# Optimization experiments

Hardware: AMD Instinct MI355X
Metric: run time of the kernel (lower is better)

## Reference

```python
import jax, jax.numpy as jnp
import numpy as np

N_SIGMA = 1
NUM_CLASS = 1
N_INST = 16          # max instance id (ids 1..16); instances==0 is background
W_INST, W_VAR, W_SEED = 1.0, 10.0, 1.0
H, W, B = 512, 512, 8
GRID = 1024          # buffer is linspace over 1024 then cropped to H,W


def make_xym(h, w, dtype=jnp.float32):
    full = jnp.linspace(0.0, 1.0, GRID, dtype=dtype)
    xm = jnp.broadcast_to(full[:w][None, :], (h, w))   # x varies along width
    ym = jnp.broadcast_to(full[:h][:, None], (h, w))   # y varies along height
    return jnp.stack([xm, ym], axis=0)                 # [2, H, W]


def lovasz_hinge_flat(logits, labels):
    # logits: [N] float, labels: [N] float in {0,1}
    signs = 2.0 * labels - 1.0
    errors = 1.0 - logits * signs
    order = jnp.argsort(-errors)
    errors_sorted = errors[order]
    gt_sorted = labels[order]
    gts = jnp.sum(gt_sorted)
    intersection = gts - jnp.cumsum(gt_sorted)
    union = gts + jnp.cumsum(1.0 - gt_sorted)
    jaccard = 1.0 - intersection / union
    grad = jnp.concatenate([jaccard[:1], jaccard[1:] - jaccard[:-1]])
    return jnp.sum(jax.nn.relu(errors_sorted) * grad)


def _per_image(pred, instance, label, xym):
    h, w = pred.shape[1], pred.shape[2]
    spatial_emb = jnp.tanh(pred[0:2]) + xym              # [2,H,W]
    sigma = pred[2:2 + N_SIGMA]                          # [n_sigma,H,W]
    seed = jax.nn.sigmoid(pred[2 + N_SIGMA])             # [H,W] (num_class==1)

    label_mask = (label == 1)
    bg_mask = (label == 0)
    seed_loss = jnp.sum(jnp.where(bg_mask, seed ** 2, 0.0))

    ids = jnp.arange(1, N_INST + 1)
    masks = (instance[None] == ids[:, None, None]) & label_mask[None]  # [K,H,W] bool
    maskf = masks.astype(pred.dtype)
    counts = jnp.sum(maskf, axis=(1, 2))                 # [K]
    present = counts > 0
    safe = jnp.maximum(counts, 1.0)

    # to_center=True: center = mean of xym coords over each instance mask
    center = jnp.einsum('khw,chw->kc', maskf, xym) / safe[:, None]        # [K,2]
    s_mean = jnp.einsum('khw,shw->ks', maskf, sigma) / safe[:, None]      # [K,n_sigma]

    # var loss: mean over in-mask pixels of (sigma - detached mean)^2
    dev2 = (sigma[None] - jax.lax.stop_gradient(s_mean)[:, :, None, None]) ** 2  # [K,ns,H,W]
    var_terms = jnp.einsum('khw,kshw->k', maskf, dev2) / (safe * N_SIGMA)

    # dist = exp(-s * sum_c (emb_c - center_c)^2), s = exp(10 * mean sigma)
    s_exp = jnp.exp(10.0 * s_mean)[:, 0]                 # [K] (n_sigma==1 broadcasts)
    diff2 = jnp.sum((spatial_emb[None] - center[:, :, None, None]) ** 2, axis=1)  # [K,H,W]
    dist = jnp.exp(-s_exp[:, None, None] * diff2)        # [K,H,W]

    inst_losses = jax.vmap(
        lambda d, m: lovasz_hinge_flat(2.0 * d.ravel() - 1.0, m.ravel())
    )(dist, maskf)
    instance_loss = jnp.sum(jnp.where(present, inst_losses, 0.0))
    var_loss = jnp.sum(jnp.where(present, var_terms, 0.0))

    seed_loss = seed_loss + jnp.sum(
        maskf * (seed[None] - jax.lax.stop_gradient(dist)) ** 2)

    obj = jnp.maximum(jnp.sum(present.astype(pred.dtype)), 1.0)
    return (W_INST * instance_loss / obj
            + W_VAR * var_loss / obj
            + W_SEED * seed_loss / (h * w))


def setup_inputs() -> dict:
    key = jax.random.key(0)
    k1, k2, k3 = jax.random.split(key, 3)
    prediction = jax.random.normal(k1, (B, 2 + N_SIGMA + NUM_CLASS, H, W), dtype=jnp.float32)
    instances = jax.random.randint(k2, (B, H, W), 0, N_INST + 1).astype(jnp.int64)
    labels = jax.random.randint(k3, (B, H, W), 0, NUM_CLASS + 1).astype(jnp.int64)
    return {"prediction": prediction, "instances": instances, "labels": labels}


def reference(prediction, instances, labels):
    xym = make_xym(prediction.shape[2], prediction.shape[3], prediction.dtype)
    per_img = jax.vmap(_per_image, in_axes=(0, 0, 0, None))(
        prediction, instances, labels, xym)
    return jnp.mean(per_img)
```

## Files before the change

### kernel.cpp

```cpp
#include <hip/hip_runtime.h>
#include <hip/hip_fp16.h>
#include <math.h>

#define HWPX 262144
#define NIMG 8
#define ACC_STRIDE 96
#define NB 1024
#define ZMAX 8.0f
#define NSPLIT 32
#define NGRP 2

typedef unsigned long long u64;

template<bool PACK>
__global__ __launch_bounds__(256) void k_prep(const float* __restrict__ pred,
    const int* __restrict__ inst, const int* __restrict__ lab,
    u64* __restrict__ rec, double* __restrict__ accd)
{
  __shared__ float s[8][83];
  int t = threadIdx.x;
  for (int i = t; i < 8*83; i += 256) (&s[0][0])[i] = 0.0f;
  __syncthreads();
  int bid = blockIdx.x;
  int b = bid >> 7;
  int base = (bid & 127) << 11;
  const float* pb = pred + (size_t)b * 4 * HWPX;
  size_t ib = (size_t)b * HWPX;
  int r = t & 7;
  float bg = 0.0f;
  #pragma unroll
  for (int i = 0; i < 8; ++i) {
    int px = base + (i << 8) + t;
    int h = px >> 9, w = px & 511;
    float xm = w * (1.0f/1023.0f), ym = h * (1.0f/1023.0f);
    float sg = pb[2*HWPX + px];
    float p3 = pb[3*HWPX + px];
    float sd = 1.0f / (1.0f + __expf(-p3));
    int lv = lab[ib+px], iv = inst[ib+px];
    int mid = (lv == 1 && (unsigned)(iv-1) < 16u) ? iv : 0;
    if (PACK) {
      float ex = tanhf(pb[px]) + xm;
      float ey = tanhf(pb[HWPX+px]) + ym;
      u64 v = (u64)__half_as_ushort(__float2half(ex))
            | ((u64)__half_as_ushort(__float2half(ey)) << 16)
            | ((u64)__half_as_ushort(__float2half(sd)) << 32)
            | ((u64)mid << 48);
      rec[ib+px] = v;
    }
    if (lv == 0) {
      bg += sd*sd;
    } else if (mid) {
      int k = mid - 1;
      atomicAdd(&s[r][k], 1.0f);
      atomicAdd(&s[r][16+k], xm);
      atomicAdd(&s[r][32+k], ym);
      atomicAdd(&s[r][48+k], sg);
      atomicAdd(&s[r][64+k], sg*sg);
    }
  }
  #pragma unroll
  for (int o = 32; o > 0; o >>= 1) bg += __shfl_down(bg, o);
  if ((t & 63) == 0) atomicAdd(&s[0][80], bg);
  __syncthreads();
  if (t < 81) {
    float v = 0.0f;
    #pragma unroll
    for (int rr = 0; rr < 8; ++rr) v += s[rr][t];
    if (v != 0.0f) atomicAdd(&accd[(size_t)b*ACC_STRIDE + t], (double)v);
  }
}

__global__ __launch_bounds__(128) void k_fin(double* __restrict__ accd, float* __restrict__ pairinfo)
{
  __shared__ double varr[128];
  __shared__ float pres[128];
  int t = threadIdx.x;
  int b = t >> 4, k = t & 15;
  double* ab = accd + (size_t)b*ACC_STRIDE;
  double cnt = ab[k];
  double safe = cnt > 0.0 ? cnt : 1.0;
  double ss = ab[48+k];
  double cx = ab[16+k]/safe, cy = ab[32+k]/safe, sm = ss/safe;
  double var = (ab[64+k] - ss*ss/safe)/safe;
  if (var < 0.0) var = 0.0;
  float4 pi = make_float4((float)cx, (float)cy, (float)exp(10.0*sm), (float)cnt);
  reinterpret_cast<float4*>(pairinfo)[t] = pi;
  pres[t] = cnt > 0.0 ? 1.0f : 0.0f;
  varr[t] = cnt > 0.0 ? var : 0.0;
  __syncthreads();
  if (t < NIMG) {
    float np = 0.0f; double vs = 0.0;
    for (int i = 0; i < 16; ++i) { np += pres[t*16+i]; vs += varr[t*16+i]; }
    double* ab2 = accd + (size_t)t*ACC_STRIDE;
    ab2[83] = vs;
    ab2[84] = (np > 1.0f) ? (double)np : 1.0;
  }
}

__global__ __launch_bounds__(1024) void k_hist(const u64* __restrict__ rec,
    const float* __restrict__ pairinfo,
    unsigned* __restrict__ partial, double* __restrict__ accd)
{
  __shared__ unsigned hist[8*NB];
  __shared__ float redf[16];
  int t = threadIdx.x, bid = blockIdx.x;
  int b = bid & 7;
  int r = bid >> 3;
  int g = r & 1;
  int s = r >> 1;
  for (int i = t; i < 8*NB; i += 1024) hist[i] = 0u;
  float cx[8], cy[8], se[8], s128[8];
  #pragma unroll
  for (int j = 0; j < 8; ++j) {
    float4 pi = reinterpret_cast<const float4*>(pairinfo)[b*16 + g*8 + j];
    cx[j] = pi.x; cy[j] = pi.y; se[j] = pi.z; s128[j] = pi.z * (float)(NB/ZMAX);
  }
  __syncthreads();
  size_t base = (size_t)b*HWPX + (size_t)s*(HWPX/NSPLIT);
  float fit = 0.0f;
  for (int it = 0; it < HWPX/NSPLIT/1024; ++it) {
    size_t px = base + it*1024 + t;
    u64 v = rec[px];
    float ex = __half2float(__ushort_as_half((unsigned short)(v & 0xffffu)));
    float ey = __half2float(__ushort_as_half((unsigned short)((v >> 16) & 0xffffu)));
    float sd = __half2float(__ushort_as_half((unsigned short)((v >> 32) & 0xffffu)));
    int rel = (int)(v >> 48) - 1 - g*8;
    #pragma unroll
    for (int j = 0; j < 8; ++j) {
      float dx = ex - cx[j], dy = ey - cy[j];
      float d2 = fmaf(dx, dx, dy*dy);
      int key; unsigned add;
      if (rel == j) {
        float d = __expf(-d2 * se[j]);
        float e = fmaf(-2.0f, d, 2.0f);
        int kk = (int)(e * (float)(NB/2));
        key = kk > NB-1 ? NB-1 : kk;
        add = 0x10000u;
        float df = sd - d; fit += df*df;
      } else {
        key = (int)fminf(d2 * s128[j], (float)(NB-1));
        add = 1u;
      }
      atomicAdd(&hist[j*NB + key], add);
    }
  }
  #pragma unroll
  for (int o = 32; o > 0; o >>= 1) fit += __shfl_down(fit, o);
  if ((t & 63) == 0) redf[t >> 6] = fit;
  __syncthreads();
  if (t == 0) {
    float ft = 0.0f;
    for (int i = 0; i < 16; ++i) ft += redf[i];
    atomicAdd(&accd[(size_t)b*ACC_STRIDE + 81], (double)ft);
  }
  unsigned* pp = partial + (size_t)((b*NGRP + g)*NSPLIT + s)*(8*NB);
  for (int i = t; i < 8*NB; i += 1024) pp[i] = hist[i];
}

__global__ __launch_bounds__(1024) void k_scan(const unsigned* __restrict__ partial,
    const float* __restrict__ pairinfo, double* __restrict__ accd)
{
  __shared__ unsigned sp[NB], sq[NB];
  __shared__ float red[16];
  int t = threadIdx.x, bid = blockIdx.x;
  int b = bid >> 4, k = bid & 15;
  int g = k >> 3, j8 = k & 7;
  float G = pairinfo[(b*16 + k)*4 + 3];
  if (G <= 0.0f) return;
  sq[t] = 0u;
  __syncthreads();
  unsigned p = 0, q = 0;
  const unsigned* basep = partial + (size_t)((b*NGRP + g)*NSPLIT)*(8*NB) + j8*NB + t;
  #pragma unroll 4
  for (int s2 = 0; s2 < NSPLIT; ++s2) {
    unsigned h = basep[(size_t)s2*(8*NB)];
    p += h >> 16; q += h & 0xffffu;
  }
  float zmid = (t + 0.5f) * (ZMAX/NB);
  float ev = 2.0f * __expf(-zmid);
  int eb = (int)(ev * (float)(NB/2));
  if (eb > NB-1) eb = NB-1;
  if (q) atomicAdd(&sq[eb], q);
  __syncthreads();
  unsigned qe = sq[t];
  __syncthreads();
  int j = (NB-1) - t;
  sp[j] = p; sq[j] = qe;
  __syncthreads();
  for (int off = 1; off < NB; off <<= 1) {
    unsigned vp = 0, vq = 0;
    if (j >= off) { vp = sp[j-off]; vq = sq[j-off]; }
    __syncthreads();
    sp[j] += vp; sq[j] += vq;
    __syncthreads();
  }
  float A  = (float)(sp[j] - p);
  float Bn = (float)(sq[j] - qe);
  float val = (t + 0.5f) * (2.0f/NB);
  float pf = (float)p, qf = (float)qe;
  float Jb = (A + Bn) / (G + Bn);
  float Ja = (A + Bn + pf + qf) / (G + Bn + qf);
  float contrib = val * (Ja - Jb);
  #pragma unroll
  for (int o = 32; o > 0; o >>= 1) contrib += __shfl_down(contrib, o);
  if ((t & 63) == 0) red[t >> 6] = contrib;
  __syncthreads();
  if (t == 0) {
    float tot = 0.0f;
    for (int i = 0; i < 16; ++i) tot += red[i];
    atomicAdd(&accd[(size_t)b*ACC_STRIDE + 82], (double)tot);
  }
}

__global__ __launch_bounds__(1024) void k_lov_old(const float* __restrict__ pred,
    const int* __restrict__ inst, const int* __restrict__ lab,
    const float* __restrict__ pairinfo, double* __restrict__ accd)
{
  constexpr int SHIFT = 18;
  constexpr int NBB = (0x40000000 >> SHIFT) + 1;
  extern __shared__ unsigned char smem[];
  unsigned* histP = reinterpret_cast<unsigned*>(smem);
  unsigned* histQ = histP + NBB;
  unsigned* scanP = histQ + NBB;
  unsigned* scanQ = scanP + 1024;
  float* red  = reinterpret_cast<float*>(scanQ + 1024);
  float* redf = red + 16;
  int t = threadIdx.x, bid = blockIdx.x;
  int b = bid >> 4, k = bid & 15;
  float4 pi = reinterpret_cast<const float4*>(pairinfo)[bid];
  float cx = pi.x, cy = pi.y, sexp = pi.z, G = pi.w;
  if (G <= 0.0f) return;
  for (int i = t; i < 2*NBB; i += 1024) histP[i] = 0u;
  __syncthreads();
  size_t ib = (size_t)b * HWPX;
  const float* pb = pred + (size_t)b * 4 * HWPX;
  const int target = k + 1;
  float fit = 0.0f;
  for (int j = 0; j < HWPX/1024; ++j) {
    int px = (j << 10) + t;
    int h = px >> 9, w = px & 511;
    float ex = tanhf(pb[px]) + w*(1.0f/1023.0f);
    float ey = tanhf(pb[HWPX+px]) + h*(1.0f/1023.0f);
    float sd = 1.0f/(1.0f + __expf(-pb[3*HWPX+px]));
    int lv = lab[ib+px], iv = inst[ib+px];
    float dx = ex - cx, dy = ey - cy;
    float d = __expf(-sexp * (dx*dx + dy*dy));
    bool m = (lv == 1) && (iv == target);
    float e = m ? fmaf(-2.0f, d, 2.0f) : 2.0f * d;
    unsigned key = __float_as_uint(e) >> SHIFT;
    atomicAdd(m ? &histP[key] : &histQ[key], 1u);
    if (m) { float df = sd - d; fit += df*df; }
  }
  #pragma unroll
  for (int o = 32; o > 0; o >>= 1) fit += __shfl_down(fit, o);
  if ((t & 63) == 0) redf[t >> 6] = fit;
  __syncthreads();
  constexpr int CB = NBB / 1024;
  int start = (NBB - 1) - t * CB;
  int nk = (t == 1023) ? (CB + 1) : CB;
  unsigned lp = 0, lq = 0;
  for (int i = 0; i < nk; ++i) { lp += histP[start-i]; lq += histQ[start-i]; }
  scanP[t] = lp; scanQ[t] = lq;
  __syncthreads();
  for (int off = 1; off < 1024; off <<= 1) {
    unsigned vp = 0, vq = 0;
    if (t >= off) { vp = scanP[t-off]; vq = scanQ[t-off]; }
    __syncthreads();
    scanP[t] += vp; scanQ[t] += vq;
    __syncthreads();
  }
  float A  = (float)(scanP[t] - lp);
  float Bn = (float)(scanQ[t] - lq);
  float contrib = 0.0f;
  for (int i = 0; i < nk; ++i) {
    int kk = start - i;
    unsigned p = histP[kk], q = histQ[kk];
    if (p | q) {
      float lo = __uint_as_float((unsigned)kk << SHIFT);
      float hi = __uint_as_float((unsigned)(kk+1) << SHIFT);
      float valv = 0.5f*(lo+hi);
      if (valv > 2.0f) valv = 2.0f;
      float pq = (float)(p + q), qf = (float)q;
      float Jb = (A + Bn) / (G + Bn);
      float Ja = (A + Bn + pq) / (G + Bn + qf);
      contrib += valv * (Ja - Jb);
      A += (float)p; Bn += qf;
    }
  }
  #pragma unroll
  for (int o = 32; o > 0; o >>= 1) contrib += __shfl_down(contrib, o);
  if ((t & 63) == 0) red[t >> 6] = contrib;
  __syncthreads();
  if (t == 0) {
    float tot = 0.0f, ft = 0.0f;
    for (int i = 0; i < 16; ++i) { tot += red[i]; ft += redf[i]; }
    atomicAdd(&accd[(size_t)b*ACC_STRIDE + 82], (double)tot);
    atomicAdd(&accd[(size_t)b*ACC_STRIDE + 81], (double)ft);
  }
}

__global__ void k_final(const double* __restrict__ accd, float* __restrict__ out)
{
  int t = threadIdx.x;
  double lb = 0.0;
  if (t < NIMG) {
    const double* ab = accd + (size_t)t*ACC_STRIDE;
    lb = (ab[82] + 10.0*ab[83]) / ab[84] + (ab[80] + ab[81]) * (1.0/(double)HWPX);
  }
  #pragma unroll
  for (int o = 4; o > 0; o >>= 1) lb += __shfl_down(lb, o);
  if (t == 0) out[0] = (float)(lb * 0.125);
}

extern "C" void kernel_launch(void* const* d_in, const int* in_sizes, int n_in,
                              void* d_out, int out_size, void* d_ws, size_t ws_size,
                              hipStream_t stream)
{
  const float* pred = (const float*)d_in[0];
  const int*   inst = (const int*)d_in[1];
  const int*   lab  = (const int*)d_in[2];
  float* out = (float*)d_out;

  size_t recB  = (size_t)NIMG * HWPX * sizeof(u64);
  size_t partB = (size_t)NIMG * NGRP * NSPLIT * 8 * NB * 4;
  size_t accB  = (size_t)NIMG * ACC_STRIDE * sizeof(double);
  size_t pairB = 128 * 4 * sizeof(float);
  bool full = ws_size >= recB + partB + accB + pairB;

  char* ws = (char*)d_ws;
  if (full) {
    u64*      rec   = (u64*)ws;
    unsigned* part  = (unsigned*)(ws + recB);
    double*   accd  = (double*)(ws + recB + partB);
    float*    pairinfo = (float*)(ws + recB + partB + accB);
    hipMemsetAsync(accd, 0, accB, stream);
    k_prep<true><<<1024,256,0,stream>>>(pred, inst, lab, rec, accd);
    k_fin<<<1,128,0,stream>>>(accd, pairinfo);
    k_hist<<<NIMG*NGRP*NSPLIT,1024,0,stream>>>(rec, pairinfo, part, accd);
    k_scan<<<128,1024,0,stream>>>(part, pairinfo, accd);
    k_final<<<1,64,0,stream>>>(accd, out);
  } else {
    double* accd = (double*)ws;
    float* pairinfo = (float*)(accd + NIMG*ACC_STRIDE);
    hipMemsetAsync(accd, 0, accB, stream);
    k_prep<false><<<1024,256,0,stream>>>(pred, inst, lab, nullptr, accd);
    k_fin<<<1,128,0,stream>>>(accd, pairinfo);
    size_t lds18 = ((size_t)2*4097 + 2048)*4 + 128;
    k_lov_old<<<128,1024,lds18,stream>>>(pred, inst, lab, pairinfo, accd);
    k_final<<<1,64,0,stream>>>(accd, out);
  }
}
```

Baseline: 72.84 us.

## Fuse finalize stages into last-block reductions and vectorize prep and histogram loads

k_fin is folded into k_prep and k_final into k_scan using an atomic ticket counter, so the last block of each grid does the cross-block reduction. This removes two kernel launches and the workspace memset. k_prep now gives each thread 8 contiguous pixels, loaded and stored as 128-bit vectors, and uses fast exp-based tanh and sigmoid. k_hist reads two records per load. Per-block stats are reduced in float rather than double atomics, and correctness depends on the ticket counter starting at a multiple of the grid size, which the code assumes without explicitly zeroing it.

Result: slower. 244.3 us (+235.5%).

```diff
diff --git a/kernel.cpp b/kernel.cpp
--- a/kernel.cpp
+++ b/kernel.cpp
@@ -9,43 +9,73 @@
 #define ZMAX 8.0f
 #define NSPLIT 32
 #define NGRP 2
+#define PREP_GRID 1024
+#define SCAN_GRID 128
 
 typedef unsigned long long u64;
+
+__device__ __forceinline__ float tanh_fast(float x) {
+  float t = __expf(2.0f * x);
+  return 1.0f - __fdividef(2.0f, t + 1.0f);
+}
+__device__ __forceinline__ float sigmoid_fast(float x) {
+  return __fdividef(1.0f, 1.0f + __expf(-x));
+}
 
 template<bool PACK>
 __global__ __launch_bounds__(256) void k_prep(const float* __restrict__ pred,
     const int* __restrict__ inst, const int* __restrict__ lab,
-    u64* __restrict__ rec, double* __restrict__ accd)
+    u64* __restrict__ rec, float* __restrict__ part,
+    double* __restrict__ accd, float* __restrict__ pairinfo, unsigned* __restrict__ tick)
 {
   __shared__ float s[8][83];
+  __shared__ float red[96];
+  __shared__ int lastFlag;
   int t = threadIdx.x;
   for (int i = t; i < 8*83; i += 256) (&s[0][0])[i] = 0.0f;
   __syncthreads();
   int bid = blockIdx.x;
   int b = bid >> 7;
-  int base = (bid & 127) << 11;
-  const float* pb = pred + (size_t)b * 4 * HWPX;
-  size_t ib = (size_t)b * HWPX;
+  int px0 = ((bid & 127) << 11) + t*8;
+  const float* pb = pred + (size_t)b*4*HWPX;
+  size_t ib = (size_t)b*HWPX;
   int r = t & 7;
+  int w0 = px0 & 511;
+  float ym = (float)(px0 >> 9) * (1.0f/1023.0f);
+
+  float4 x0 = *(const float4*)(pb + px0);
+  float4 x1 = *(const float4*)(pb + px0 + 4);
+  float4 y0 = *(const float4*)(pb + HWPX + px0);
+  float4 y1 = *(const float4*)(pb + HWPX + px0 + 4);
+  float4 g0 = *(const float4*)(pb + 2*HWPX + px0);
+  float4 g1 = *(const float4*)(pb + 2*HWPX + px0 + 4);
+  float4 q0 = *(const float4*)(pb + 3*HWPX + px0);
+  float4 q1 = *(const float4*)(pb + 3*HWPX + px0 + 4);
+  int4 l0 = *(const int4*)(lab + ib + px0);
+  int4 l1 = *(const int4*)(lab + ib + px0 + 4);
+  int4 i0 = *(const int4*)(inst + ib + px0);
+  int4 i1 = *(const int4*)(inst + ib + px0 + 4);
+  float xs[8] = {x0.x,x0.y,x0.z,x0.w,x1.x,x1.y,x1.z,x1.w};
+  float ys[8] = {y0.x,y0.y,y0.z,y0.w,y1.x,y1.y,y1.z,y1.w};
+  float gs[8] = {g0.x,g0.y,g0.z,g0.w,g1.x,g1.y,g1.z,g1.w};
+  float qs[8] = {q0.x,q0.y,q0.z,q0.w,q1.x,q1.y,q1.z,q1.w};
+  int   ls[8] = {l0.x,l0.y,l0.z,l0.w,l1.x,l1.y,l1.z,l1.w};
+  int   is[8] = {i0.x,i0.y,i0.z,i0.w,i1.x,i1.y,i1.z,i1.w};
+  u64 rv[8];
   float bg = 0.0f;
   #pragma unroll
   for (int i = 0; i < 8; ++i) {
-    int px = base + (i << 8) + t;
-    int h = px >> 9, w = px & 511;
-    float xm = w * (1.0f/1023.0f), ym = h * (1.0f/1023.0f);
-    float sg = pb[2*HWPX + px];
-    float p3 = pb[3*HWPX + px];
-    float sd = 1.0f / (1.0f + __expf(-p3));
-    int lv = lab[ib+px], iv = inst[ib+px];
+    float xm = (float)(w0 + i) * (1.0f/1023.0f);
+    float sd = sigmoid_fast(qs[i]);
+    int lv = ls[i], iv = is[i];
     int mid = (lv == 1 && (unsigned)(iv-1) < 16u) ? iv : 0;
     if (PACK) {
-      float ex = tanhf(pb[px]) + xm;
-      float ey = tanhf(pb[HWPX+px]) + ym;
-      u64 v = (u64)__half_as_ushort(__float2half(ex))
+      float ex = tanh_fast(xs[i]) + xm;
+      float ey = tanh_fast(ys[i]) + ym;
+      rv[i] = (u64)__half_as_ushort(__float2half(ex))
             | ((u64)__half_as_ushort(__float2half(ey)) << 16)
             | ((u64)__half_as_ushort(__float2half(sd)) << 32)
             | ((u64)mid << 48);
-      rec[ib+px] = v;
     }
     if (lv == 0) {
       bg += sd*sd;
@@ -54,46 +84,73 @@
       atomicAdd(&s[r][k], 1.0f);
       atomicAdd(&s[r][16+k], xm);
       atomicAdd(&s[r][32+k], ym);
-      atomicAdd(&s[r][48+k], sg);
-      atomicAdd(&s[r][64+k], sg*sg);
-    }
+      atomicAdd(&s[r][48+k], gs[i]);
+      atomicAdd(&s[r][64+k], gs[i]*gs[i]);
+    }
+  }
+  if (PACK) {
+    ulonglong2* rp = (ulonglong2*)(rec + ib + px0);
+    rp[0] = make_ulonglong2(rv[0], rv[1]);
+    rp[1] = make_ulonglong2(rv[2], rv[3]);
+    rp[2] = make_ulonglong2(rv[4], rv[5]);
+    rp[3] = make_ulonglong2(rv[6], rv[7]);
   }
   #pragma unroll
   for (int o = 32; o > 0; o >>= 1) bg += __shfl_down(bg, o);
   if ((t & 63) == 0) atomicAdd(&s[0][80], bg);
   __syncthreads();
-  if (t < 81) {
+  if (t < 96) {
     float v = 0.0f;
-    #pragma unroll
-    for (int rr = 0; rr < 8; ++rr) v += s[rr][t];
-    if (v != 0.0f) atomicAdd(&accd[(size_t)b*ACC_STRIDE + t], (double)v);
-  }
-}
-
-__global__ __launch_bounds__(128) void k_fin(double* __restrict__ accd, float* __restrict__ pairinfo)
-{
-  __shared__ double varr[128];
-  __shared__ float pres[128];
-  int t = threadIdx.x;
-  int b = t >> 4, k = t & 15;
-  double* ab = accd + (size_t)b*ACC_STRIDE;
-  double cnt = ab[k];
-  double safe = cnt > 0.0 ? cnt : 1.0;
-  double ss = ab[48+k];
-  double cx = ab[16+k]/safe, cy = ab[32+k]/safe, sm = ss/safe;
-  double var = (ab[64+k] - ss*ss/safe)/safe;
-  if (var < 0.0) var = 0.0;
-  float4 pi = make_float4((float)cx, (float)cy, (float)exp(10.0*sm), (float)cnt);
-  reinterpret_cast<float4*>(pairinfo)[t] = pi;
-  pres[t] = cnt > 0.0 ? 1.0f : 0.0f;
-  varr[t] = cnt > 0.0 ? var : 0.0;
-  __syncthreads();
-  if (t < NIMG) {
-    float np = 0.0f; double vs = 0.0;
-    for (int i = 0; i < 16; ++i) { np += pres[t*16+i]; vs += varr[t*16+i]; }
-    double* ab2 = accd + (size_t)t*ACC_STRIDE;
-    ab2[83] = vs;
-    ab2[84] = (np > 1.0f) ? (double)np : 1.0;
+    if (t < 83) {
+      #pragma unroll
+      for (int rr = 0; rr < 8; ++rr) v += s[rr][t];
+    }
+    part[(size_t)bid*96 + t] = v;
+  }
+  __threadfence();
+  if (t == 0) {
+    unsigned old = atomicAdd(tick, 1u);
+    lastFlag = ((old & (unsigned)(PREP_GRID-1)) == (unsigned)(PREP_GRID-1)) ? 1 : 0;
+  }
+  __syncthreads();
+  if (!lastFlag) return;
+  __threadfence();
+  for (int b2 = 0; b2 < NIMG; ++b2) {
+    if (t < 96) {
+      float v = 0.0f;
+      const float* pp = part + (size_t)b2*128*96 + t;
+      #pragma unroll 8
+      for (int blk = 0; blk < 128; ++blk) v += pp[(size_t)blk*96];
+      red[t] = v;
+    }
+    __syncthreads();
+    if (t < 16) {
+      float cnt = red[t];
+      float safe = cnt > 0.0f ? cnt : 1.0f;
+      float sm = red[48+t] / safe;
+      float4 pi = make_float4(red[16+t]/safe, red[32+t]/safe, __expf(10.0f*sm), cnt);
+      ((float4*)pairinfo)[b2*16 + t] = pi;
+    }
+    if (t == 0) {
+      double vs = 0.0; float np = 0.0f;
+      for (int k2 = 0; k2 < 16; ++k2) {
+        float cnt = red[k2];
+        if (cnt > 0.0f) {
+          np += 1.0f;
+          float ssg = red[48+k2];
+          float var = (red[64+k2] - ssg*ssg/cnt) / cnt;
+          if (var < 0.0f) var = 0.0f;
+          vs += (double)var;
+        }
+      }
+      double* ab = accd + (size_t)b2*ACC_STRIDE;
+      ab[80] = (double)red[80];
+      ab[81] = 0.0;
+      ab[82] = 0.0;
+      ab[83] = vs;
+      ab[84] = np > 1.0f ? (double)np : 1.0;
+    }
+    __syncthreads();
   }
 }
 
@@ -105,43 +162,48 @@
   __shared__ float redf[16];
   int t = threadIdx.x, bid = blockIdx.x;
   int b = bid & 7;
-  int r = bid >> 3;
-  int g = r & 1;
-  int s = r >> 1;
+  int rr = bid >> 3;
+  int g = rr & 1;
+  int s = rr >> 1;
   for (int i = t; i < 8*NB; i += 1024) hist[i] = 0u;
   float cx[8], cy[8], se[8], s128[8];
   #pragma unroll
   for (int j = 0; j < 8; ++j) {
-    float4 pi = reinterpret_cast<const float4*>(pairinfo)[b*16 + g*8 + j];
+    float4 pi = ((const float4*)pairinfo)[b*16 + g*8 + j];
     cx[j] = pi.x; cy[j] = pi.y; se[j] = pi.z; s128[j] = pi.z * (float)(NB/ZMAX);
   }
   __syncthreads();
   size_t base = (size_t)b*HWPX + (size_t)s*(HWPX/NSPLIT);
   float fit = 0.0f;
-  for (int it = 0; it < HWPX/NSPLIT/1024; ++it) {
-    size_t px = base + it*1024 + t;
-    u64 v = rec[px];
-    float ex = __half2float(__ushort_as_half((unsigned short)(v & 0xffffu)));
-    float ey = __half2float(__ushort_as_half((unsigned short)((v >> 16) & 0xffffu)));
-    float sd = __half2float(__ushort_as_half((unsigned short)((v >> 32) & 0xffffu)));
-    int rel = (int)(v >> 48) - 1 - g*8;
+  for (int it = 0; it < HWPX/NSPLIT/2048; ++it) {
+    size_t px = base + it*2048 + t*2;
+    ulonglong2 v2 = *((const ulonglong2*)(rec + px));
+    u64 vv[2] = {v2.x, v2.y};
     #pragma unroll
-    for (int j = 0; j < 8; ++j) {
-      float dx = ex - cx[j], dy = ey - cy[j];
-      float d2 = fmaf(dx, dx, dy*dy);
-      int key; unsigned add;
-      if (rel == j) {
-        float d = __expf(-d2 * se[j]);
-        float e = fmaf(-2.0f, d, 2.0f);
-        int kk = (int)(e * (float)(NB/2));
-        key = kk > NB-1 ? NB-1 : kk;
-        add = 0x10000u;
-        float df = sd - d; fit += df*df;
-      } else {
-        key = (int)fminf(d2 * s128[j], (float)(NB-1));
-        add = 1u;
+    for (int c = 0; c < 2; ++c) {
+      u64 v = vv[c];
+      float ex = __half2float(__ushort_as_half((unsigned short)(v & 0xffffu)));
+      float ey = __half2float(__ushort_as_half((unsigned short)((v >> 16) & 0xffffu)));
+      float sd = __half2float(__ushort_as_half((unsigned short)((v >> 32) & 0xffffu)));
+      int rel = (int)(v >> 48) - 1 - g*8;
+      #pragma unroll
+      for (int j = 0; j < 8; ++j) {
+        float dx = ex - cx[j], dy = ey - cy[j];
+        float d2 = fmaf(dx, dx, dy*dy);
+        int key; unsigned add;
+        if (rel == j) {
+          float d = __expf(-d2 * se[j]);
+          float e = fmaf(-2.0f, d, 2.0f);
+          int kk = (int)(e * (float)(NB/2));
+          key = kk > NB-1 ? NB-1 : kk;
+          add = 0x10000u;
+          float df = sd - d; fit += df*df;
+        } else {
+          key = (int)fminf(d2 * s128[j], (float)(NB-1));
+          add = 1u;
+        }
+        atomicAdd(&hist[j*NB + key], add);
       }
-      atomicAdd(&hist[j*NB + key], add);
     }
   }
   #pragma unroll
@@ -158,57 +220,78 @@
 }
 
 __global__ __launch_bounds__(1024) void k_scan(const unsigned* __restrict__ partial,
-    const float* __restrict__ pairinfo, double* __restrict__ accd)
+    const float* __restrict__ pairinfo, double* __restrict__ accd,
+    float* __restrict__ out, unsigned* __restrict__ tick)
 {
   __shared__ unsigned sp[NB], sq[NB];
   __shared__ float red[16];
+  __shared__ int lastFlag;
   int t = threadIdx.x, bid = blockIdx.x;
   int b = bid >> 4, k = bid & 15;
   int g = k >> 3, j8 = k & 7;
   float G = pairinfo[(b*16 + k)*4 + 3];
-  if (G <= 0.0f) return;
-  sq[t] = 0u;
-  __syncthreads();
-  unsigned p = 0, q = 0;
-  const unsigned* basep = partial + (size_t)((b*NGRP + g)*NSPLIT)*(8*NB) + j8*NB + t;
-  #pragma unroll 4
-  for (int s2 = 0; s2 < NSPLIT; ++s2) {
-    unsigned h = basep[(size_t)s2*(8*NB)];
-    p += h >> 16; q += h & 0xffffu;
-  }
-  float zmid = (t + 0.5f) * (ZMAX/NB);
-  float ev = 2.0f * __expf(-zmid);
-  int eb = (int)(ev * (float)(NB/2));
-  if (eb > NB-1) eb = NB-1;
-  if (q) atomicAdd(&sq[eb], q);
-  __syncthreads();
-  unsigned qe = sq[t];
-  __syncthreads();
-  int j = (NB-1) - t;
-  sp[j] = p; sq[j] = qe;
-  __syncthreads();
-  for (int off = 1; off < NB; off <<= 1) {
-    unsigned vp = 0, vq = 0;
-    if (j >= off) { vp = sp[j-off]; vq = sq[j-off]; }
-    __syncthreads();
-    sp[j] += vp; sq[j] += vq;
-    __syncthreads();
-  }
-  float A  = (float)(sp[j] - p);
-  float Bn = (float)(sq[j] - qe);
-  float val = (t + 0.5f) * (2.0f/NB);
-  float pf = (float)p, qf = (float)qe;
-  float Jb = (A + Bn) / (G + Bn);
-  float Ja = (A + Bn + pf + qf) / (G + Bn + qf);
-  float contrib = val * (Ja - Jb);
-  #pragma unroll
-  for (int o = 32; o > 0; o >>= 1) contrib += __shfl_down(contrib, o);
-  if ((t & 63) == 0) red[t >> 6] = contrib;
-  __syncthreads();
+  if (G > 0.0f) {
+    sq[t] = 0u;
+    __syncthreads();
+    unsigned p = 0, q = 0;
+    const unsigned* basep = partial + (size_t)((b*NGRP + g)*NSPLIT)*(8*NB) + j8*NB + t;
+    #pragma unroll 4
+    for (int s2 = 0; s2 < NSPLIT; ++s2) {
+      unsigned h = basep[(size_t)s2*(8*NB)];
+      p += h >> 16; q += h & 0xffffu;
+    }
+    float zmid = (t + 0.5f) * (ZMAX/NB);
+    float ev = 2.0f * __expf(-zmid);
+    int eb = (int)(ev * (float)(NB/2));
+    if (eb > NB-1) eb = NB-1;
+    if (q) atomicAdd(&sq[eb], q);
+    __syncthreads();
+    unsigned qe = sq[t];
+    __syncthreads();
+    int j = (NB-1) - t;
+    sp[j] = p; sq[j] = qe;
+    __syncthreads();
+    for (int off = 1; off < NB; off <<= 1) {
+      unsigned vp = 0, vq = 0;
+      if (j >= off) { vp = sp[j-off]; vq = sq[j-off]; }
+      __syncthreads();
+      sp[j] += vp; sq[j] += vq;
+      __syncthreads();
+    }
+    float A  = (float)(sp[j] - p);
+    float Bn = (float)(sq[j] - qe);
+    float val = (t + 0.5f) * (2.0f/NB);
+    float pf = (float)p, qf = (float)qe;
+    float Jb = (A + Bn) / (G + Bn);
+    float Ja = (A + Bn + pf + qf) / (G + Bn + qf);
+    float contrib = val * (Ja - Jb);
+    #pragma unroll
+    for (int o = 32; o > 0; o >>= 1) contrib += __shfl_down(contrib, o);
+    if ((t & 63) == 0) red[t >> 6] = contrib;
+    __syncthreads();
+    if (t == 0) {
+      float tot = 0.0f;
+      for (int i = 0; i < 16; ++i) tot += red[i];
+      atomicAdd(&accd[(size_t)b*ACC_STRIDE + 82], (double)tot);
+    }
+  }
+  __threadfence();
   if (t == 0) {
-    float tot = 0.0f;
-    for (int i = 0; i < 16; ++i) tot += red[i];
-    atomicAdd(&accd[(size_t)b*ACC_STRIDE + 82], (double)tot);
+    unsigned old = atomicAdd(tick, 1u);
+    lastFlag = ((old & (unsigned)(SCAN_GRID-1)) == (unsigned)(SCAN_GRID-1)) ? 1 : 0;
+  }
+  __syncthreads();
+  if (!lastFlag) return;
+  __threadfence();
+  double lb = 0.0;
+  if (t < NIMG) {
+    const double* ab = accd + (size_t)t*ACC_STRIDE;
+    lb = (ab[82] + 10.0*ab[83]) / ab[84] + (ab[80] + ab[81]) * (1.0/(double)HWPX);
+  }
+  if (t < 64) {
+    #pragma unroll
+    for (int o = 4; o > 0; o >>= 1) lb += __shfl_down(lb, o);
+    if (t == 0) out[0] = (float)(lb * 0.125);
   }
 }
 
@@ -321,30 +404,31 @@
   const int*   lab  = (const int*)d_in[2];
   float* out = (float*)d_out;
 
-  size_t recB  = (size_t)NIMG * HWPX * sizeof(u64);
-  size_t partB = (size_t)NIMG * NGRP * NSPLIT * 8 * NB * 4;
-  size_t accB  = (size_t)NIMG * ACC_STRIDE * sizeof(double);
-  size_t pairB = 128 * 4 * sizeof(float);
-  bool full = ws_size >= recB + partB + accB + pairB;
+  size_t recB   = (size_t)NIMG * HWPX * sizeof(u64);
+  size_t partB  = (size_t)NIMG * NGRP * NSPLIT * 8 * NB * 4;
+  size_t pstatB = (size_t)PREP_GRID * 96 * sizeof(float);
+  size_t accB   = (size_t)NIMG * ACC_STRIDE * sizeof(double);
+  size_t pairB  = 128 * 4 * sizeof(float);
+  size_t tickB  = 64;
+  bool full = ws_size >= recB + partB + pstatB + accB + pairB + tickB;
 
   char* ws = (char*)d_ws;
   if (full) {
     u64*      rec   = (u64*)ws;
     unsigned* part  = (unsigned*)(ws + recB);
-    double*   accd  = (double*)(ws + recB + partB);
-    float*    pairinfo = (float*)(ws + recB + partB + accB);
-    hipMemsetAsync(accd, 0, accB, stream);
-    k_prep<true><<<1024,256,0,stream>>>(pred, inst, lab, rec, accd);
-    k_fin<<<1,128,0,stream>>>(accd, pairinfo);
+    float*    pstat = (float*)(ws + recB + partB);
+    double*   accd  = (double*)(ws + recB + partB + pstatB);
+    float*    pairinfo = (float*)(ws + recB + partB + pstatB + accB);
+    unsigned* tick  = (unsigned*)(ws + recB + partB + pstatB + accB + pairB);
+    k_prep<true><<<PREP_GRID,256,0,stream>>>(pred, inst, lab, rec, pstat, accd, pairinfo, tick);
     k_hist<<<NIMG*NGRP*NSPLIT,1024,0,stream>>>(rec, pairinfo, part, accd);
-    k_scan<<<128,1024,0,stream>>>(part, pairinfo, accd);
-    k_final<<<1,64,0,stream>>>(accd, out);
+    k_scan<<<SCAN_GRID,1024,0,stream>>>(part, pairinfo, accd, out, tick+1);
   } else {
-    double* accd = (double*)ws;
-    float* pairinfo = (float*)(accd + NIMG*ACC_STRIDE);
-    hipMemsetAsync(accd, 0, accB, stream);
-    k_prep<false><<<1024,256,0,stream>>>(pred, inst, lab, nullptr, accd);
-    k_fin<<<1,128,0,stream>>>(accd, pairinfo);
+    float*    pstat = (float*)ws;
+    double*   accd  = (double*)(ws + pstatB);
+    float*    pairinfo = (float*)(ws + pstatB + accB);
+    unsigned* tick  = (unsigned*)(ws + pstatB + accB + pairB);
+    k_prep<false><<<PREP_GRID,256,0,stream>>>(pred, inst, lab, nullptr, pstat, accd, pairinfo, tick);
     size_t lds18 = ((size_t)2*4097 + 2048)*4 + 128;
     k_lov_old<<<128,1024,lds18,stream>>>(pred, inst, lab, pairinfo, accd);
     k_final<<<1,64,0,stream>>>(accd, out);
```
